# Optimization experiments

Hardware: AMD Instinct MI355X
Metric: run time of the kernel (lower is better)

The kernel has to match this reference:

```python
import jax, jax.numpy as jnp
import numpy as np

CHUNK = 256  # rows of the distance matrix materialized at a time


def _min_sq_dist(x, y):
    """For each point in x [N,3], squared distance to nearest point in y [M,3].
    Computed tile-by-tile via lax.scan so the full [N,M] matrix is never built.
    Matches pytorch3d knn_points(K=1).dists (squared Euclidean)."""
    n = x.shape[0]
    x2 = jnp.sum(x * x, axis=-1)            # [N]
    y2 = jnp.sum(y * y, axis=-1)            # [M]
    xs = x.reshape(n // CHUNK, CHUNK, 3)
    x2s = x2.reshape(n // CHUNK, CHUNK)

    def body(carry, inp):
        xc, x2c = inp                        # [C,3], [C]
        d = x2c[:, None] + y2[None, :] - 2.0 * (xc @ y.T)
        return carry, jnp.min(d, axis=1)     # [C]

    _, mins = jax.lax.scan(body, None, (xs, x2s))
    return mins.reshape(-1)                  # [N]


def setup_inputs() -> dict:
    key = jax.random.key(0)
    k1, k2 = jax.random.split(key)
    pred = jax.random.normal(k1, (131072, 4), dtype=jnp.float32)
    target = jax.random.normal(k2, (131072, 4), dtype=jnp.float32)
    return {"pred": pred, "target": target}


def reference(pred, target):
    loss_weight = 1.0
    p = pred[:, :3]
    t = target[:, :3]
    min_p2t = _min_sq_dist(p, t)   # adv_KNN: pred -> target
    min_t2p = _min_sq_dist(t, p)   # ori_KNN: target -> pred
    chamfer = jnp.mean(min_p2t) + jnp.mean(min_t2p)
    return chamfer * loss_weight
```

## Files before the change

### kernel.cpp

```cpp
#include <hip/hip_runtime.h>


#define G 128
#define GSH 7
#define CCELLS (G * G * G)
#define H 0.1f
#define INVH 10.0f
#define ORIG (-6.4f)
#define NCHUNK (CCELLS / 256)
#define SSTRIDE 2097168u
#define INFB 3.4e38f

__device__ __forceinline__ int cellcoord(float x) {
    int c = (int)floorf((x - ORIG) * INVH);
    return min(max(c, 0), G - 1);
}
__device__ __forceinline__ int cellof(float x, float y, float z) {
    return (cellcoord(z) << (2 * GSH)) + (cellcoord(y) << GSH) + cellcoord(x);
}
__device__ __forceinline__ float axdist(int u, float qc) {
    float lo = ORIG + u * H;
    float dlo = (u == 0) ? 0.0f : lo - qc;
    float dhi = (u == G - 1) ? 0.0f : qc - (lo + H);
    return fmaxf(0.0f, fmaxf(dlo, dhi));
}
__device__ __forceinline__ float scan_run(
    const float4* __restrict__ pts, unsigned int k, unsigned int ke,
    float cx, float cy, float cz, float lbest) {
    for (; k < ke; ++k) {
        float4 ya = pts[k];
        lbest = fminf(lbest, fmaf(cx, ya.x, fmaf(cy, ya.y, fmaf(cz, ya.z, ya.w))));
    }
    return lbest;
}

__global__ __launch_bounds__(256) void hist2_kernel(
    const float4* __restrict__ A, const float4* __restrict__ B,
    unsigned int* __restrict__ counts, int n) {
    int i = blockIdx.x * 256 + threadIdx.x;
    const float4* in = blockIdx.y ? B : A;
    unsigned int* c = counts + blockIdx.y * CCELLS;
    if (i < n) {
        float4 a = in[i];
        atomicAdd(&c[cellof(a.x, a.y, a.z)], 1u);
    }
}

__global__ __launch_bounds__(256) void scan_chunk2_kernel(
    const unsigned int* __restrict__ counts, unsigned int* __restrict__ excl,
    unsigned int* __restrict__ blockSums) {
    __shared__ unsigned int lds[256];
    int cb = blockIdx.x & (NCHUNK - 1);
    int b = blockIdx.x >> 13;
    int g = cb * 256 + threadIdx.x;
    unsigned int v = counts[b * CCELLS + g];
    lds[threadIdx.x] = v;
    __syncthreads();
    for (int off = 1; off < 256; off <<= 1) {
        unsigned int t = (threadIdx.x >= off) ? lds[threadIdx.x - off] : 0u;
        __syncthreads();
        lds[threadIdx.x] += t;
        __syncthreads();
    }
    excl[b * SSTRIDE + g] = lds[threadIdx.x] - v;
    if (threadIdx.x == 255) blockSums[blockIdx.x] = lds[255];
}

__global__ __launch_bounds__(256) void scan_sums2_kernel(
    unsigned int* __restrict__ bs0) {
    unsigned int* bs = bs0 + blockIdx.x * NCHUNK;
    __shared__ unsigned int lds[256];
    int t = threadIdx.x;
    unsigned int s = 0;
    for (int k = 0; k < NCHUNK / 256; ++k) s += bs[t * (NCHUNK / 256) + k];
    lds[t] = s;
    __syncthreads();
    for (int off = 1; off < 256; off <<= 1) {
        unsigned int u = (t >= off) ? lds[t - off] : 0u;
        __syncthreads();
        lds[t] += u;
        __syncthreads();
    }
    unsigned int run = lds[t] - s;
    for (int k = 0; k < NCHUNK / 256; ++k) {
        unsigned int v = bs[t * (NCHUNK / 256) + k];
        bs[t * (NCHUNK / 256) + k] = run;
        run += v;
    }
}

__global__ __launch_bounds__(256) void add_offsets2_kernel(
    unsigned int* __restrict__ excl, unsigned int* __restrict__ next,
    const unsigned int* __restrict__ bs, int n) {
    int cb = blockIdx.x & (NCHUNK - 1);
    int b = blockIdx.x >> 13;
    int g = cb * 256 + threadIdx.x;
    unsigned int v = excl[b * SSTRIDE + g] + bs[blockIdx.x];
    excl[b * SSTRIDE + g] = v;
    next[b * CCELLS + g] = v;
    if (g == 0) excl[b * SSTRIDE + CCELLS] = (unsigned int)n;
}

__global__ __launch_bounds__(256) void scatter2_kernel(
    const float4* __restrict__ A, const float4* __restrict__ B,
    unsigned int* __restrict__ next, float4* __restrict__ sorted, int n) {
    int i = blockIdx.x * 256 + threadIdx.x;
    const float4* in = blockIdx.y ? B : A;
    unsigned int* nx = next + blockIdx.y * CCELLS;
    float4* out = sorted + blockIdx.y * n;
    if (i < n) {
        float4 a = in[i];
        unsigned int slot = atomicAdd(&nx[cellof(a.x, a.y, a.z)], 1u);
        float s = fmaf(a.x, a.x, fmaf(a.y, a.y, a.z * a.z));
        out[slot] = make_float4(a.x, a.y, a.z, s);
    }
}

__global__ __launch_bounds__(256) void nn_pass1_kernel(
    const float4* __restrict__ sortedPT, const unsigned int* __restrict__ startPT,
    int n, unsigned int* __restrict__ wlPT, unsigned int* __restrict__ wbPT,
    unsigned int* __restrict__ cnts, double* __restrict__ acc) {
    int dir = blockIdx.y;
    const float4* Q = sortedPT + (size_t)dir * n;
    const float4* pts = sortedPT + (size_t)(1 - dir) * n;
    const unsigned int* start = startPT + (size_t)(1 - dir) * SSTRIDE;
    unsigned int* wl = wlPT + (size_t)dir * n;
    unsigned int* wb = wbPT + (size_t)dir * n;
    unsigned int* cnt = cnts + dir;

    int i = blockIdx.x * 256 + threadIdx.x;
    float v = 0.0f;
    if (i < n) {
        float4 q = Q[i];
        float cx = -2.0f * q.x, cy = -2.0f * q.y, cz = -2.0f * q.z;
        float q2 = q.w;
        int qx = cellcoord(q.x), qy = cellcoord(q.y), qz = cellcoord(q.z);
        int x0 = max(qx - 1, 0), x1 = min(qx + 1, G - 1);
        unsigned int ss[9], ee[9];
        int idx = 0;
#pragma unroll
        for (int dz = -1; dz <= 1; ++dz) {
            int uz = min(max(qz + dz, 0), G - 1);
#pragma unroll
            for (int dy = -1; dy <= 1; ++dy) {
                int uy = min(max(qy + dy, 0), G - 1);
                unsigned int base = ((unsigned)uz << (2 * GSH)) + ((unsigned)uy << GSH);
                ss[idx] = start[base + x0];
                ee[idx] = start[base + x1 + 1];
                ++idx;
            }
        }
        float best = 3.4e38f;
#pragma unroll
        for (int r = 0; r < 9; ++r) {
            unsigned int k = ss[r], e = ee[r];
            for (; k + 2 <= e; k += 2) {
                float4 ya = pts[k];
                float4 yb = pts[k + 1];
                float ea = fmaf(cx, ya.x, fmaf(cy, ya.y, fmaf(cz, ya.z, ya.w)));
                float eb = fmaf(cx, yb.x, fmaf(cy, yb.y, fmaf(cz, yb.z, yb.w)));
                best = fminf(fminf(best, ea), eb);
            }
            if (k < e) {
                float4 ya = pts[k];
                best = fminf(best, fmaf(cx, ya.x, fmaf(cy, ya.y, fmaf(cz, ya.z, ya.w))));
            }
        }
        float ba = q2 + best;
        float fx = q.x - (ORIG + (float)qx * H);
        float fy = q.y - (ORIG + (float)qy * H);
        float fz = q.z - (ORIG + (float)qz * H);
        float bx = fminf((qx >= 2) ? (fx + H) : INFB,
                         (qx <= G - 3) ? (2.0f * H - fx) : INFB);
        float by = fminf((qy >= 2) ? (fy + H) : INFB,
                         (qy <= G - 3) ? (2.0f * H - fy) : INFB);
        float bz = fminf((qz >= 2) ? (fz + H) : INFB,
                         (qz <= G - 3) ? (2.0f * H - fz) : INFB);
        float bound = fminf(bx, fminf(by, bz)) * 0.99999f;
        if (ba <= bound * bound) {
            v = ba;
        } else {
            unsigned int w = atomicAdd(cnt, 1u);
            wl[w] = (unsigned int)i;
            wb[w] = __float_as_uint(best);
        }
    }
    for (int off = 32; off > 0; off >>= 1) v += __shfl_down(v, off);
    __shared__ float partial[4];
    int lane = threadIdx.x & 63, wid = threadIdx.x >> 6;
    if (lane == 0) partial[wid] = v;
    __syncthreads();
    if (threadIdx.x == 0)
        atomicAdd(acc, (double)((partial[0] + partial[1]) + (partial[2] + partial[3])));
}

__global__ __launch_bounds__(256) void nn_pass2_kernel(
    const float4* __restrict__ sortedPT, const unsigned int* __restrict__ startPT,
    int n, const unsigned int* __restrict__ wlPT, const unsigned int* __restrict__ wbPT,
    const unsigned int* __restrict__ cnts, double* __restrict__ acc) {
    int dir = blockIdx.y;
    const float4* Q = sortedPT + (size_t)dir * n;
    const float4* pts = sortedPT + (size_t)(1 - dir) * n;
    const unsigned int* start = startPT + (size_t)(1 - dir) * SSTRIDE;
    const unsigned int* wl = wlPT + (size_t)dir * n;
    const unsigned int* wb = wbPT + (size_t)dir * n;
    unsigned int m = cnts[dir];

    int lane = threadIdx.x & 63;
    int gwave = (blockIdx.x * 256 + threadIdx.x) >> 6;
    int nwave = gridDim.x * 4;
    float wsum = 0.0f;
    for (unsigned int e = gwave; e < m; e += (unsigned int)nwave) {
        unsigned int qi = wl[e];
        float4 q = Q[qi];
        float cx = -2.0f * q.x, cy = -2.0f * q.y, cz = -2.0f * q.z;
        float q2 = q.w;
        int qx = cellcoord(q.x), qy = cellcoord(q.y), qz = cellcoord(q.z);
        float fx = q.x - (ORIG + (float)qx * H);
        float fy = q.y - (ORIG + (float)qy * H);
        float fz = q.z - (ORIG + (float)qz * H);
        float best = __uint_as_float(wb[e]);
        int Rp = 1;
        int Rb = 2;
        for (;;) {
            int z0 = max(qz - Rb, 0), z1 = min(qz + Rb, G - 1);
            int y0 = max(qy - Rb, 0), y1 = min(qy + Rb, G - 1);
            int x0 = max(qx - Rb, 0), x1 = min(qx + Rb, G - 1);
            int nyr = y1 - y0 + 1;
            int nrows = (z1 - z0 + 1) * nyr;
            float lbest = best;
            for (int r = lane; r < nrows; r += 64) {
                int uz = z0 + r / nyr;
                int uy = y0 + r % nyr;
                int az = uz > qz ? uz - qz : qz - uz;
                int ay = uy > qy ? uy - qy : qy - uy;
                float dz = axdist(uz, q.z), dy = axdist(uy, q.y);
                float rowd2 = fmaf(dz, dz, dy * dy);
                if (rowd2 >= q2 + lbest) continue;
                unsigned int base = ((unsigned)uz << (2 * GSH)) + ((unsigned)uy << GSH);
                if (az <= Rp && ay <= Rp) {
                    int xa1 = qx - Rp - 1;
                    int xb0 = qx + Rp + 1;
                    if (xa1 >= x0)
                        lbest = scan_run(pts, start[base + x0], start[base + xa1 + 1],
                                         cx, cy, cz, lbest);
                    if (xb0 <= x1)
                        lbest = scan_run(pts, start[base + xb0], start[base + x1 + 1],
                                         cx, cy, cz, lbest);
                } else {
                    lbest = scan_run(pts, start[base + x0], start[base + x1 + 1],
                                     cx, cy, cz, lbest);
                }
            }
            for (int off = 32; off > 0; off >>= 1)
                lbest = fminf(lbest, __shfl_xor(lbest, off));
            best = lbest;
            float bx = fminf((qx - Rb >= 1) ? fmaf((float)Rb, H, fx) : INFB,
                             (qx + Rb + 1 <= G - 1) ? ((float)(Rb + 1) * H - fx) : INFB);
            float by = fminf((qy - Rb >= 1) ? fmaf((float)Rb, H, fy) : INFB,
                             (qy + Rb + 1 <= G - 1) ? ((float)(Rb + 1) * H - fy) : INFB);
            float bz = fminf((qz - Rb >= 1) ? fmaf((float)Rb, H, fz) : INFB,
                             (qz + Rb + 1 <= G - 1) ? ((float)(Rb + 1) * H - fz) : INFB);
            float bound = fminf(bx, fminf(by, bz)) * 0.99999f;
            if (q2 + best <= bound * bound || Rb >= G) break;
            Rp = Rb;
            Rb = min(Rb * 2, G);
        }
        wsum += q2 + best;
    }
    if (lane == 0 && wsum != 0.0f) atomicAdd(acc, (double)wsum);
}

__global__ void finalize_kernel(const double* __restrict__ acc,
                                float* __restrict__ out, int n) {
    out[0] = (float)(acc[0] / (double)n);
}

#define SPLIT 16
#define PTS 4
__global__ __launch_bounds__(256) void pack_kernel(
    const float4* __restrict__ in, float4* __restrict__ out, int n) {
    int i = blockIdx.x * 256 + threadIdx.x;
    if (i < n) {
        float4 a = in[i];
        float s = fmaf(a.x, a.x, fmaf(a.y, a.y, a.z * a.z));
        out[i] = make_float4(a.x, a.y, a.z, s);
    }
}
__device__ __forceinline__ unsigned int enc_f32(float f) {
    unsigned int u = __float_as_uint(f);
    return (u & 0x80000000u) ? ~u : (u | 0x80000000u);
}
__device__ __forceinline__ float dec_f32(unsigned int u) {
    u = (u & 0x80000000u) ? (u ^ 0x80000000u) : ~u;
    return __uint_as_float(u);
}
__global__ __launch_bounds__(256) void chamfer_dir_kernel(
    const float4* __restrict__ X, const float4* __restrict__ Y,
    int m, unsigned int* __restrict__ mins) {
    int base = blockIdx.x * (256 * PTS) + threadIdx.x;
    float x2x[PTS], x2y[PTS], x2z[PTS], xw[PTS], mn[PTS];
#pragma unroll
    for (int p = 0; p < PTS; ++p) {
        float4 x = X[base + p * 256];
        x2x[p] = -2.0f * x.x; x2y[p] = -2.0f * x.y; x2z[p] = -2.0f * x.z;
        xw[p] = x.w; mn[p] = 3.4e38f;
    }
    int seglen = m / SPLIT, j0 = blockIdx.y * seglen, j1 = j0 + seglen;
    for (int j = j0; j < j1; j += 8) {
#pragma unroll
        for (int u = 0; u < 8; u += 2) {
            float4 ya = Y[j + u];
            float4 yb = Y[j + u + 1];
#pragma unroll
            for (int p = 0; p < PTS; ++p) {
                float ea = fmaf(x2x[p], ya.x, fmaf(x2y[p], ya.y, fmaf(x2z[p], ya.z, ya.w)));
                float eb = fmaf(x2x[p], yb.x, fmaf(x2y[p], yb.y, fmaf(x2z[p], yb.z, yb.w)));
                mn[p] = fminf(fminf(mn[p], ea), eb);
            }
        }
    }
#pragma unroll
    for (int p = 0; p < PTS; ++p)
        atomicMin(&mins[base + p * 256], enc_f32(xw[p] + mn[p]));
}
__global__ __launch_bounds__(256) void reduce_kernel(
    const unsigned int* __restrict__ mins, int total, double* __restrict__ acc) {
    float s = 0.0f;
    for (int i = blockIdx.x * 256 + threadIdx.x; i < total; i += gridDim.x * 256)
        s += dec_f32(mins[i]);
    for (int off = 32; off > 0; off >>= 1) s += __shfl_down(s, off);
    __shared__ float partial[4];
    int lane = threadIdx.x & 63, wid = threadIdx.x >> 6;
    if (lane == 0) partial[wid] = s;
    __syncthreads();
    if (threadIdx.x == 0)
        atomicAdd(acc, (double)((partial[0] + partial[1]) + (partial[2] + partial[3])));
}

extern "C" void kernel_launch(void* const* d_in, const int* in_sizes, int n_in,
                              void* d_out, int out_size, void* d_ws, size_t ws_size,
                              hipStream_t stream) {
    const float4* pred = (const float4*)d_in[0];
    const float4* targ = (const float4*)d_in[1];
    float* out = (float*)d_out;
    int n = in_sizes[0] / 4;
    int nblk = (n + 255) / 256;

    char* ws = (char*)d_ws;
    double* acc = (double*)ws;
    unsigned int* cnts = (unsigned int*)(ws + 8);

    size_t startB = (size_t)SSTRIDE * 4;
    size_t needGrid = 64 + 2 * startB + 2ull * CCELLS * 4 + 2ull * n * 16
                    + 4ull * n * 4 + 2ull * NCHUNK * 4;

    if (ws_size >= needGrid && n == 131072) {
        char* p = ws + 64;
        unsigned int* startPT = (unsigned int*)p;  p += 2 * startB;
        unsigned int* nextPT = (unsigned int*)p;   p += 2ull * CCELLS * 4;
        float4* sortedPT = (float4*)p;             p += 2ull * n * 16;
        unsigned int* wlPT = (unsigned int*)p;     p += 2ull * n * 4;
        unsigned int* wbPT = (unsigned int*)p;     p += 2ull * n * 4;
        unsigned int* blockSums = (unsigned int*)p;

        hipMemsetAsync(ws, 0, 16, stream);
        hipMemsetAsync(nextPT, 0, 2ull * CCELLS * 4, stream);
        hist2_kernel<<<dim3(nblk, 2), 256, 0, stream>>>(pred, targ, nextPT, n);
        scan_chunk2_kernel<<<2 * NCHUNK, 256, 0, stream>>>(nextPT, startPT, blockSums);
        scan_sums2_kernel<<<2, 256, 0, stream>>>(blockSums);
        add_offsets2_kernel<<<2 * NCHUNK, 256, 0, stream>>>(startPT, nextPT, blockSums, n);
        scatter2_kernel<<<dim3(nblk, 2), 256, 0, stream>>>(pred, targ, nextPT, sortedPT, n);

        nn_pass1_kernel<<<dim3(nblk, 2), 256, 0, stream>>>(
            sortedPT, startPT, n, wlPT, wbPT, cnts, acc);
        nn_pass2_kernel<<<dim3(512, 2), 256, 0, stream>>>(
            sortedPT, startPT, n, wlPT, wbPT, cnts, acc);
    } else {
        hipMemsetAsync(acc, 0, sizeof(double), stream);
        size_t needBF = 64 + 2ull * n * sizeof(float4) + 2ull * n * sizeof(unsigned int);
        if (ws_size >= needBF && (n % (256 * PTS)) == 0 && (n % SPLIT) == 0) {
            float4* P = (float4*)(ws + 64);
            float4* T = P + n;
            unsigned int* minPT = (unsigned int*)(T + n);
            pack_kernel<<<nblk, 256, 0, stream>>>(pred, P, n);
            pack_kernel<<<nblk, 256, 0, stream>>>(targ, T, n);
            hipMemsetAsync(minPT, 0xFF, 2ull * n * sizeof(unsigned int), stream);
            dim3 grid(n / (256 * PTS), SPLIT);
            chamfer_dir_kernel<<<grid, 256, 0, stream>>>(P, T, n, minPT);
            chamfer_dir_kernel<<<grid, 256, 0, stream>>>(T, P, n, minPT + n);
            reduce_kernel<<<256, 256, 0, stream>>>(minPT, 2 * n, acc);
        }
    }
    finalize_kernel<<<1, 1, 0, stream>>>(acc, out, n);
}
```

Measured before the change: 259.6 us.

## Add cell-occupancy bitmask to skip empty rows and dynamic work dequeue in pass2

The histogram kernel now also sets one bit per occupied grid cell in a 64-bit-word bitmap. In the second NN pass, each row of cells is checked against that bitmap, and rows with no points in the x range are skipped before any start-index loads. The strided wave-to-query assignment is replaced by an atomic work queue, so waves pull fallback queries dynamically and uneven search radii balance out. The cost is an extra memset and an atomicOr per point, plus one global atomic per query in pass2.

Result: slower. 455.8 us (+75.6%).

```diff
diff --git a/kernel.cpp b/kernel.cpp
--- a/kernel.cpp
+++ b/kernel.cpp
@@ -9,6 +9,7 @@
 #define ORIG (-6.4f)
 #define NCHUNK (CCELLS / 256)
 #define SSTRIDE 2097168u
+#define OCCW (CCELLS / 64)
 #define INFB 3.4e38f
 
 __device__ __forceinline__ int cellcoord(float x) {
@@ -33,16 +34,23 @@
     }
     return lbest;
 }
+__device__ __forceinline__ unsigned long long rmask(int lo, int hi) {
+    return ((hi - lo == 63) ? ~0ull : (((1ull << (hi - lo + 1)) - 1ull) << lo));
+}
 
 __global__ __launch_bounds__(256) void hist2_kernel(
     const float4* __restrict__ A, const float4* __restrict__ B,
-    unsigned int* __restrict__ counts, int n) {
+    unsigned int* __restrict__ counts, unsigned long long* __restrict__ occ,
+    int n) {
     int i = blockIdx.x * 256 + threadIdx.x;
     const float4* in = blockIdx.y ? B : A;
     unsigned int* c = counts + blockIdx.y * CCELLS;
+    unsigned long long* oc = occ + blockIdx.y * OCCW;
     if (i < n) {
         float4 a = in[i];
-        atomicAdd(&c[cellof(a.x, a.y, a.z)], 1u);
+        int cell = cellof(a.x, a.y, a.z);
+        atomicAdd(&c[cell], 1u);
+        atomicOr(&oc[cell >> 6], 1ull << (cell & 63));
     }
 }
 
@@ -196,21 +204,27 @@
 
 __global__ __launch_bounds__(256) void nn_pass2_kernel(
     const float4* __restrict__ sortedPT, const unsigned int* __restrict__ startPT,
+    const unsigned long long* __restrict__ occPT,
     int n, const unsigned int* __restrict__ wlPT, const unsigned int* __restrict__ wbPT,
-    const unsigned int* __restrict__ cnts, double* __restrict__ acc) {
+    const unsigned int* __restrict__ cnts, unsigned int* __restrict__ deqs,
+    double* __restrict__ acc) {
     int dir = blockIdx.y;
     const float4* Q = sortedPT + (size_t)dir * n;
     const float4* pts = sortedPT + (size_t)(1 - dir) * n;
     const unsigned int* start = startPT + (size_t)(1 - dir) * SSTRIDE;
+    const unsigned long long* occ = occPT + (size_t)(1 - dir) * OCCW;
     const unsigned int* wl = wlPT + (size_t)dir * n;
     const unsigned int* wb = wbPT + (size_t)dir * n;
+    unsigned int* deq = deqs + dir;
     unsigned int m = cnts[dir];
 
     int lane = threadIdx.x & 63;
-    int gwave = (blockIdx.x * 256 + threadIdx.x) >> 6;
-    int nwave = gridDim.x * 4;
     float wsum = 0.0f;
-    for (unsigned int e = gwave; e < m; e += (unsigned int)nwave) {
+    for (;;) {
+        unsigned int e = 0;
+        if (lane == 0) e = atomicAdd(deq, 1u);
+        e = __shfl(e, 0);
+        if (e >= m) break;
         unsigned int qi = wl[e];
         float4 q = Q[qi];
         float cx = -2.0f * q.x, cy = -2.0f * q.y, cz = -2.0f * q.z;
@@ -238,6 +252,13 @@
                 float rowd2 = fmaf(dz, dz, dy * dy);
                 if (rowd2 >= q2 + lbest) continue;
                 unsigned int base = ((unsigned)uz << (2 * GSH)) + ((unsigned)uy << GSH);
+                {
+                    unsigned int w0 = base >> 6;
+                    unsigned long long a = 0;
+                    if (x0 < 64) a = occ[w0] & rmask(x0, min(x1, 63));
+                    if (x1 >= 64) a |= occ[w0 + 1] & rmask(max(x0, 64) - 64, x1 - 64);
+                    if (!a) continue;
+                }
                 if (az <= Rp && ay <= Rp) {
                     int xa1 = qx - Rp - 1;
                     int xb0 = qx + Rp + 1;
@@ -350,23 +371,26 @@
     char* ws = (char*)d_ws;
     double* acc = (double*)ws;
     unsigned int* cnts = (unsigned int*)(ws + 8);
+    unsigned int* deqs = (unsigned int*)(ws + 16);
 
     size_t startB = (size_t)SSTRIDE * 4;
     size_t needGrid = 64 + 2 * startB + 2ull * CCELLS * 4 + 2ull * n * 16
-                    + 4ull * n * 4 + 2ull * NCHUNK * 4;
+                    + 4ull * n * 4 + 2ull * OCCW * 8 + 2ull * NCHUNK * 4;
 
     if (ws_size >= needGrid && n == 131072) {
         char* p = ws + 64;
-        unsigned int* startPT = (unsigned int*)p;  p += 2 * startB;
-        unsigned int* nextPT = (unsigned int*)p;   p += 2ull * CCELLS * 4;
-        float4* sortedPT = (float4*)p;             p += 2ull * n * 16;
-        unsigned int* wlPT = (unsigned int*)p;     p += 2ull * n * 4;
-        unsigned int* wbPT = (unsigned int*)p;     p += 2ull * n * 4;
+        unsigned int* startPT = (unsigned int*)p;        p += 2 * startB;
+        unsigned int* nextPT = (unsigned int*)p;         p += 2ull * CCELLS * 4;
+        float4* sortedPT = (float4*)p;                   p += 2ull * n * 16;
+        unsigned int* wlPT = (unsigned int*)p;           p += 2ull * n * 4;
+        unsigned int* wbPT = (unsigned int*)p;           p += 2ull * n * 4;
+        unsigned long long* occPT = (unsigned long long*)p; p += 2ull * OCCW * 8;
         unsigned int* blockSums = (unsigned int*)p;
 
-        hipMemsetAsync(ws, 0, 16, stream);
+        hipMemsetAsync(ws, 0, 64, stream);
         hipMemsetAsync(nextPT, 0, 2ull * CCELLS * 4, stream);
-        hist2_kernel<<<dim3(nblk, 2), 256, 0, stream>>>(pred, targ, nextPT, n);
+        hipMemsetAsync(occPT, 0, 2ull * OCCW * 8, stream);
+        hist2_kernel<<<dim3(nblk, 2), 256, 0, stream>>>(pred, targ, nextPT, occPT, n);
         scan_chunk2_kernel<<<2 * NCHUNK, 256, 0, stream>>>(nextPT, startPT, blockSums);
         scan_sums2_kernel<<<2, 256, 0, stream>>>(blockSums);
         add_offsets2_kernel<<<2 * NCHUNK, 256, 0, stream>>>(startPT, nextPT, blockSums, n);
@@ -375,7 +399,7 @@
         nn_pass1_kernel<<<dim3(nblk, 2), 256, 0, stream>>>(
             sortedPT, startPT, n, wlPT, wbPT, cnts, acc);
         nn_pass2_kernel<<<dim3(512, 2), 256, 0, stream>>>(
-            sortedPT, startPT, n, wlPT, wbPT, cnts, acc);
+            sortedPT, startPT, occPT, n, wlPT, wbPT, cnts, deqs, acc);
     } else {
         hipMemsetAsync(acc, 0, sizeof(double), stream);
         size_t needBF = 64 + 2ull * n * sizeof(float4) + 2ull * n * sizeof(unsigned int);
```

## Add coarse 32^3 grid for pass-2 nearest-neighbor fallback search

Applied to the files above, without the earlier changes.

Builds a second, coarser uniform grid (32^3 cells of size 0.4) alongside the fine 128^3 grid, with its own histogram, scan and scatter into a reused buffer. The fallback pass-2 search for unresolved queries now walks this coarse grid, growing the search shell by one cell at a time instead of doubling on the fine grid. The aim is fewer cell-start lookups and row iterations for far-away outlier queries. The cost is the extra sort kernels and atomics in the build phase.

After: 316.5 us. 21.9% more time.

```diff
diff --git a/kernel.cpp b/kernel.cpp
--- a/kernel.cpp
+++ b/kernel.cpp
@@ -9,6 +9,15 @@
 #define ORIG (-6.4f)
 #define NCHUNK (CCELLS / 256)
 #define SSTRIDE 2097168u
+
+#define G2 32
+#define GSH2 5
+#define CCELLS2 (G2 * G2 * G2)
+#define H2 0.4f
+#define INVH2 2.5f
+#define NCHUNK2 (CCELLS2 / 256)
+#define SSTRIDE2 32784u
+
 #define INFB 3.4e38f
 
 __device__ __forceinline__ int cellcoord(float x) {
@@ -18,10 +27,17 @@
 __device__ __forceinline__ int cellof(float x, float y, float z) {
     return (cellcoord(z) << (2 * GSH)) + (cellcoord(y) << GSH) + cellcoord(x);
 }
-__device__ __forceinline__ float axdist(int u, float qc) {
-    float lo = ORIG + u * H;
+__device__ __forceinline__ int cellcoord2(float x) {
+    int c = (int)floorf((x - ORIG) * INVH2);
+    return min(max(c, 0), G2 - 1);
+}
+__device__ __forceinline__ int cellof2(float x, float y, float z) {
+    return (cellcoord2(z) << (2 * GSH2)) + (cellcoord2(y) << GSH2) + cellcoord2(x);
+}
+__device__ __forceinline__ float axdist2(int u, float qc) {
+    float lo = ORIG + u * H2;
     float dlo = (u == 0) ? 0.0f : lo - qc;
-    float dhi = (u == G - 1) ? 0.0f : qc - (lo + H);
+    float dhi = (u == G2 - 1) ? 0.0f : qc - (lo + H2);
     return fmaxf(0.0f, fmaxf(dlo, dhi));
 }
 __device__ __forceinline__ float scan_run(
@@ -36,13 +52,16 @@
 
 __global__ __launch_bounds__(256) void hist2_kernel(
     const float4* __restrict__ A, const float4* __restrict__ B,
-    unsigned int* __restrict__ counts, int n) {
+    unsigned int* __restrict__ counts, unsigned int* __restrict__ counts2,
+    int n) {
     int i = blockIdx.x * 256 + threadIdx.x;
     const float4* in = blockIdx.y ? B : A;
     unsigned int* c = counts + blockIdx.y * CCELLS;
+    unsigned int* c2 = counts2 + blockIdx.y * CCELLS2;
     if (i < n) {
         float4 a = in[i];
         atomicAdd(&c[cellof(a.x, a.y, a.z)], 1u);
+        atomicAdd(&c2[cellof2(a.x, a.y, a.z)], 1u);
     }
 }
 
@@ -111,6 +130,69 @@
     if (i < n) {
         float4 a = in[i];
         unsigned int slot = atomicAdd(&nx[cellof(a.x, a.y, a.z)], 1u);
+        float s = fmaf(a.x, a.x, fmaf(a.y, a.y, a.z * a.z));
+        out[slot] = make_float4(a.x, a.y, a.z, s);
+    }
+}
+
+__global__ __launch_bounds__(256) void scan_chunk2c_kernel(
+    const unsigned int* __restrict__ counts2, unsigned int* __restrict__ excl2,
+    unsigned int* __restrict__ blockSums2) {
+    __shared__ unsigned int lds[256];
+    int cb = blockIdx.x & (NCHUNK2 - 1);
+    int b = blockIdx.x >> 7;
+    int g = cb * 256 + threadIdx.x;
+    unsigned int v = counts2[b * CCELLS2 + g];
+    lds[threadIdx.x] = v;
+    __syncthreads();
+    for (int off = 1; off < 256; off <<= 1) {
+        unsigned int t = (threadIdx.x >= off) ? lds[threadIdx.x - off] : 0u;
+        __syncthreads();
+        lds[threadIdx.x] += t;
+        __syncthreads();
+    }
+    excl2[b * SSTRIDE2 + g] = lds[threadIdx.x] - v;
+    if (threadIdx.x == 255) blockSums2[blockIdx.x] = lds[255];
+}
+
+__global__ void scan_sums2c_kernel(unsigned int* __restrict__ bs0) {
+    unsigned int* bs = bs0 + blockIdx.x * NCHUNK2;
+    __shared__ unsigned int lds[NCHUNK2];
+    int t = threadIdx.x;
+    unsigned int v = bs[t];
+    lds[t] = v;
+    __syncthreads();
+    for (int off = 1; off < NCHUNK2; off <<= 1) {
+        unsigned int u = (t >= off) ? lds[t - off] : 0u;
+        __syncthreads();
+        lds[t] += u;
+        __syncthreads();
+    }
+    bs[t] = lds[t] - v;
+}
+
+__global__ __launch_bounds__(256) void add_offsets2c_kernel(
+    unsigned int* __restrict__ excl2, unsigned int* __restrict__ next2,
+    const unsigned int* __restrict__ bs2, int n) {
+    int cb = blockIdx.x & (NCHUNK2 - 1);
+    int b = blockIdx.x >> 7;
+    int g = cb * 256 + threadIdx.x;
+    unsigned int v = excl2[b * SSTRIDE2 + g] + bs2[blockIdx.x];
+    excl2[b * SSTRIDE2 + g] = v;
+    next2[b * CCELLS2 + g] = v;
+    if (g == 0) excl2[b * SSTRIDE2 + CCELLS2] = (unsigned int)n;
+}
+
+__global__ __launch_bounds__(256) void scatter2c_kernel(
+    const float4* __restrict__ A, const float4* __restrict__ B,
+    unsigned int* __restrict__ next2, float4* __restrict__ sortedC, int n) {
+    int i = blockIdx.x * 256 + threadIdx.x;
+    const float4* in = blockIdx.y ? B : A;
+    unsigned int* nx = next2 + blockIdx.y * CCELLS2;
+    float4* out = sortedC + blockIdx.y * n;
+    if (i < n) {
+        float4 a = in[i];
+        unsigned int slot = atomicAdd(&nx[cellof2(a.x, a.y, a.z)], 1u);
         float s = fmaf(a.x, a.x, fmaf(a.y, a.y, a.z * a.z));
         out[slot] = make_float4(a.x, a.y, a.z, s);
     }
@@ -195,13 +277,14 @@
 }
 
 __global__ __launch_bounds__(256) void nn_pass2_kernel(
-    const float4* __restrict__ sortedPT, const unsigned int* __restrict__ startPT,
+    const float4* __restrict__ sortedPT, const float4* __restrict__ sortedC,
+    const unsigned int* __restrict__ startC,
     int n, const unsigned int* __restrict__ wlPT, const unsigned int* __restrict__ wbPT,
     const unsigned int* __restrict__ cnts, double* __restrict__ acc) {
     int dir = blockIdx.y;
     const float4* Q = sortedPT + (size_t)dir * n;
-    const float4* pts = sortedPT + (size_t)(1 - dir) * n;
-    const unsigned int* start = startPT + (size_t)(1 - dir) * SSTRIDE;
+    const float4* pts = sortedC + (size_t)(1 - dir) * n;
+    const unsigned int* start = startC + (size_t)(1 - dir) * SSTRIDE2;
     const unsigned int* wl = wlPT + (size_t)dir * n;
     const unsigned int* wb = wbPT + (size_t)dir * n;
     unsigned int m = cnts[dir];
@@ -215,17 +298,17 @@
         float4 q = Q[qi];
         float cx = -2.0f * q.x, cy = -2.0f * q.y, cz = -2.0f * q.z;
         float q2 = q.w;
-        int qx = cellcoord(q.x), qy = cellcoord(q.y), qz = cellcoord(q.z);
-        float fx = q.x - (ORIG + (float)qx * H);
-        float fy = q.y - (ORIG + (float)qy * H);
-        float fz = q.z - (ORIG + (float)qz * H);
+        int qx = cellcoord2(q.x), qy = cellcoord2(q.y), qz = cellcoord2(q.z);
+        float fx = q.x - (ORIG + (float)qx * H2);
+        float fy = q.y - (ORIG + (float)qy * H2);
+        float fz = q.z - (ORIG + (float)qz * H2);
         float best = __uint_as_float(wb[e]);
-        int Rp = 1;
-        int Rb = 2;
+        int Rp = -1;
+        int Rb = 1;
         for (;;) {
-            int z0 = max(qz - Rb, 0), z1 = min(qz + Rb, G - 1);
-            int y0 = max(qy - Rb, 0), y1 = min(qy + Rb, G - 1);
-            int x0 = max(qx - Rb, 0), x1 = min(qx + Rb, G - 1);
+            int z0 = max(qz - Rb, 0), z1 = min(qz + Rb, G2 - 1);
+            int y0 = max(qy - Rb, 0), y1 = min(qy + Rb, G2 - 1);
+            int x0 = max(qx - Rb, 0), x1 = min(qx + Rb, G2 - 1);
             int nyr = y1 - y0 + 1;
             int nrows = (z1 - z0 + 1) * nyr;
             float lbest = best;
@@ -234,10 +317,10 @@
                 int uy = y0 + r % nyr;
                 int az = uz > qz ? uz - qz : qz - uz;
                 int ay = uy > qy ? uy - qy : qy - uy;
-                float dz = axdist(uz, q.z), dy = axdist(uy, q.y);
+                float dz = axdist2(uz, q.z), dy = axdist2(uy, q.y);
                 float rowd2 = fmaf(dz, dz, dy * dy);
                 if (rowd2 >= q2 + lbest) continue;
-                unsigned int base = ((unsigned)uz << (2 * GSH)) + ((unsigned)uy << GSH);
+                unsigned int base = ((unsigned)uz << (2 * GSH2)) + ((unsigned)uy << GSH2);
                 if (az <= Rp && ay <= Rp) {
                     int xa1 = qx - Rp - 1;
                     int xb0 = qx + Rp + 1;
@@ -255,16 +338,16 @@
             for (int off = 32; off > 0; off >>= 1)
                 lbest = fminf(lbest, __shfl_xor(lbest, off));
             best = lbest;
-            float bx = fminf((qx - Rb >= 1) ? fmaf((float)Rb, H, fx) : INFB,
-                             (qx + Rb + 1 <= G - 1) ? ((float)(Rb + 1) * H - fx) : INFB);
-            float by = fminf((qy - Rb >= 1) ? fmaf((float)Rb, H, fy) : INFB,
-                             (qy + Rb + 1 <= G - 1) ? ((float)(Rb + 1) * H - fy) : INFB);
-            float bz = fminf((qz - Rb >= 1) ? fmaf((float)Rb, H, fz) : INFB,
-                             (qz + Rb + 1 <= G - 1) ? ((float)(Rb + 1) * H - fz) : INFB);
+            float bx = fminf((qx - Rb >= 1) ? fmaf((float)Rb, H2, fx) : INFB,
+                             (qx + Rb + 1 <= G2 - 1) ? ((float)(Rb + 1) * H2 - fx) : INFB);
+            float by = fminf((qy - Rb >= 1) ? fmaf((float)Rb, H2, fy) : INFB,
+                             (qy + Rb + 1 <= G2 - 1) ? ((float)(Rb + 1) * H2 - fy) : INFB);
+            float bz = fminf((qz - Rb >= 1) ? fmaf((float)Rb, H2, fz) : INFB,
+                             (qz + Rb + 1 <= G2 - 1) ? ((float)(Rb + 1) * H2 - fz) : INFB);
             float bound = fminf(bx, fminf(by, bz)) * 0.99999f;
-            if (q2 + best <= bound * bound || Rb >= G) break;
+            if (q2 + best <= bound * bound || Rb >= G2) break;
             Rp = Rb;
-            Rb = min(Rb * 2, G);
+            Rb += 1;
         }
         wsum += q2 + best;
     }
@@ -352,30 +435,40 @@
     unsigned int* cnts = (unsigned int*)(ws + 8);
 
     size_t startB = (size_t)SSTRIDE * 4;
-    size_t needGrid = 64 + 2 * startB + 2ull * CCELLS * 4 + 2ull * n * 16
-                    + 4ull * n * 4 + 2ull * NCHUNK * 4;
+    size_t startB2 = (size_t)SSTRIDE2 * 4;
+    size_t needGrid = 64 + 2 * startB + 2ull * CCELLS * 4 + 2ull * CCELLS2 * 4
+                    + 2 * startB2 + 2ull * n * 16 + 4ull * n * 4
+                    + 2ull * NCHUNK * 4 + 2ull * NCHUNK2 * 4;
 
     if (ws_size >= needGrid && n == 131072) {
         char* p = ws + 64;
         unsigned int* startPT = (unsigned int*)p;  p += 2 * startB;
         unsigned int* nextPT = (unsigned int*)p;   p += 2ull * CCELLS * 4;
+        unsigned int* nextC = (unsigned int*)p;    p += 2ull * CCELLS2 * 4;
+        unsigned int* startC = (unsigned int*)p;   p += 2 * startB2;
         float4* sortedPT = (float4*)p;             p += 2ull * n * 16;
         unsigned int* wlPT = (unsigned int*)p;     p += 2ull * n * 4;
         unsigned int* wbPT = (unsigned int*)p;     p += 2ull * n * 4;
-        unsigned int* blockSums = (unsigned int*)p;
-
-        hipMemsetAsync(ws, 0, 16, stream);
-        hipMemsetAsync(nextPT, 0, 2ull * CCELLS * 4, stream);
-        hist2_kernel<<<dim3(nblk, 2), 256, 0, stream>>>(pred, targ, nextPT, n);
+        unsigned int* blockSums = (unsigned int*)p; p += 2ull * NCHUNK * 4;
+        unsigned int* blockSums2 = (unsigned int*)p;
+        float4* sortedC = (float4*)nextPT;
+
+        hipMemsetAsync(ws, 0, 64, stream);
+        hipMemsetAsync(nextPT, 0, 2ull * CCELLS * 4 + 2ull * CCELLS2 * 4, stream);
+        hist2_kernel<<<dim3(nblk, 2), 256, 0, stream>>>(pred, targ, nextPT, nextC, n);
         scan_chunk2_kernel<<<2 * NCHUNK, 256, 0, stream>>>(nextPT, startPT, blockSums);
         scan_sums2_kernel<<<2, 256, 0, stream>>>(blockSums);
         add_offsets2_kernel<<<2 * NCHUNK, 256, 0, stream>>>(startPT, nextPT, blockSums, n);
         scatter2_kernel<<<dim3(nblk, 2), 256, 0, stream>>>(pred, targ, nextPT, sortedPT, n);
+        scan_chunk2c_kernel<<<2 * NCHUNK2, 256, 0, stream>>>(nextC, startC, blockSums2);
+        scan_sums2c_kernel<<<2, NCHUNK2, 0, stream>>>(blockSums2);
+        add_offsets2c_kernel<<<2 * NCHUNK2, 256, 0, stream>>>(startC, nextC, blockSums2, n);
+        scatter2c_kernel<<<dim3(nblk, 2), 256, 0, stream>>>(pred, targ, nextC, sortedC, n);
 
         nn_pass1_kernel<<<dim3(nblk, 2), 256, 0, stream>>>(
             sortedPT, startPT, n, wlPT, wbPT, cnts, acc);
         nn_pass2_kernel<<<dim3(512, 2), 256, 0, stream>>>(
-            sortedPT, startPT, n, wlPT, wbPT, cnts, acc);
+            sortedPT, sortedC, startC, n, wlPT, wbPT, cnts, acc);
     } else {
         hipMemsetAsync(acc, 0, sizeof(double), stream);
         size_t needBF = 64 + 2ull * n * sizeof(float4) + 2ull * n * sizeof(unsigned int);
```

## Use two-level grid: small fine grid for pass1, coarse grid for pass2 fallback

Applied to the files above, without the earlier changes.

Replaces the single 128^3 fine grid spanning [-6.4,6.4] with a 64^3 fine grid over [-3.2,3.2] for the 3x3x3 first pass, plus a 32^3 coarse grid with 0.4 cell size for the second pass. This shrinks the histogram, scan and offset work over millions of mostly empty cells, and the fine points are clamped to the boundary cells outside the central region. Pass 2 now starts its search radius from the pass-1 best distance and grows it by one coarse cell per step instead of doubling, and it launches twice as many blocks. The cost is a second scatter into a second sorted copy, plus more points clamped into edge cells, which can send more queries to the slower pass 2.

Result: slower. 736.4 us (+183.7%).

```diff
diff --git a/kernel.cpp b/kernel.cpp
--- a/kernel.cpp
+++ b/kernel.cpp
@@ -1,27 +1,44 @@
 #include <hip/hip_runtime.h>
 
 
-#define G 128
-#define GSH 7
-#define CCELLS (G * G * G)
-#define H 0.1f
-#define INVH 10.0f
-#define ORIG (-6.4f)
-#define NCHUNK (CCELLS / 256)
-#define SSTRIDE 2097168u
+#define GF 64
+#define GSHF 6
+#define CCF (GF * GF * GF)
+#define HF 0.1f
+#define INVHF 10.0f
+#define ORIGF (-3.2f)
+#define NCHF (CCF / 256)
+#define SSF 262160u
+
+#define G2 32
+#define GSH2 5
+#define CC2 (G2 * G2 * G2)
+#define H2 0.4f
+#define INVH2 2.5f
+#define ORIG2 (-6.4f)
+#define NCH2 (CC2 / 256)
+#define SS2 32784u
+
 #define INFB 3.4e38f
 
-__device__ __forceinline__ int cellcoord(float x) {
-    int c = (int)floorf((x - ORIG) * INVH);
-    return min(max(c, 0), G - 1);
-}
-__device__ __forceinline__ int cellof(float x, float y, float z) {
-    return (cellcoord(z) << (2 * GSH)) + (cellcoord(y) << GSH) + cellcoord(x);
-}
-__device__ __forceinline__ float axdist(int u, float qc) {
-    float lo = ORIG + u * H;
+__device__ __forceinline__ int cellcoordF(float x) {
+    int c = (int)floorf((x - ORIGF) * INVHF);
+    return min(max(c, 0), GF - 1);
+}
+__device__ __forceinline__ int cellofF(float x, float y, float z) {
+    return (cellcoordF(z) << (2 * GSHF)) + (cellcoordF(y) << GSHF) + cellcoordF(x);
+}
+__device__ __forceinline__ int cellcoord2(float x) {
+    int c = (int)floorf((x - ORIG2) * INVH2);
+    return min(max(c, 0), G2 - 1);
+}
+__device__ __forceinline__ int cellof2(float x, float y, float z) {
+    return (cellcoord2(z) << (2 * GSH2)) + (cellcoord2(y) << GSH2) + cellcoord2(x);
+}
+__device__ __forceinline__ float axdist2(int u, float qc) {
+    float lo = ORIG2 + u * H2;
     float dlo = (u == 0) ? 0.0f : lo - qc;
-    float dhi = (u == G - 1) ? 0.0f : qc - (lo + H);
+    float dhi = (u == G2 - 1) ? 0.0f : qc - (lo + H2);
     return fmaxf(0.0f, fmaxf(dlo, dhi));
 }
 __device__ __forceinline__ float scan_run(
@@ -36,24 +53,45 @@
 
 __global__ __launch_bounds__(256) void hist2_kernel(
     const float4* __restrict__ A, const float4* __restrict__ B,
-    unsigned int* __restrict__ counts, int n) {
+    unsigned int* __restrict__ countsF, unsigned int* __restrict__ countsC,
+    int n) {
     int i = blockIdx.x * 256 + threadIdx.x;
     const float4* in = blockIdx.y ? B : A;
-    unsigned int* c = counts + blockIdx.y * CCELLS;
+    unsigned int* cF = countsF + (size_t)blockIdx.y * CCF;
+    unsigned int* cC = countsC + (size_t)blockIdx.y * CC2;
     if (i < n) {
         float4 a = in[i];
-        atomicAdd(&c[cellof(a.x, a.y, a.z)], 1u);
-    }
-}
-
-__global__ __launch_bounds__(256) void scan_chunk2_kernel(
-    const unsigned int* __restrict__ counts, unsigned int* __restrict__ excl,
-    unsigned int* __restrict__ blockSums) {
+        atomicAdd(&cF[cellofF(a.x, a.y, a.z)], 1u);
+        atomicAdd(&cC[cellof2(a.x, a.y, a.z)], 1u);
+    }
+}
+
+__global__ __launch_bounds__(256) void scan_chunk_all_kernel(
+    const unsigned int* __restrict__ countsF, unsigned int* __restrict__ exclF,
+    unsigned int* __restrict__ bsF,
+    const unsigned int* __restrict__ countsC, unsigned int* __restrict__ exclC,
+    unsigned int* __restrict__ bsC) {
     __shared__ unsigned int lds[256];
-    int cb = blockIdx.x & (NCHUNK - 1);
-    int b = blockIdx.x >> 13;
-    int g = cb * 256 + threadIdx.x;
-    unsigned int v = counts[b * CCELLS + g];
+    int bid = blockIdx.x;
+    const unsigned int* cnt;
+    unsigned int* excl;
+    unsigned int* bsp;
+    int g;
+    if (bid < 2 * NCHF) {
+        int b = bid >> 10, cb = bid & (NCHF - 1);
+        g = cb * 256 + threadIdx.x;
+        cnt = countsF + (size_t)b * CCF;
+        excl = exclF + (size_t)b * SSF;
+        bsp = bsF + bid;
+    } else {
+        int b2 = bid - 2 * NCHF;
+        int b = b2 >> 7, cb = b2 & (NCH2 - 1);
+        g = cb * 256 + threadIdx.x;
+        cnt = countsC + (size_t)b * CC2;
+        excl = exclC + (size_t)b * SS2;
+        bsp = bsC + b2;
+    }
+    unsigned int v = cnt[g];
     lds[threadIdx.x] = v;
     __syncthreads();
     for (int off = 1; off < 256; off <<= 1) {
@@ -62,68 +100,99 @@
         lds[threadIdx.x] += t;
         __syncthreads();
     }
-    excl[b * SSTRIDE + g] = lds[threadIdx.x] - v;
-    if (threadIdx.x == 255) blockSums[blockIdx.x] = lds[255];
-}
-
-__global__ __launch_bounds__(256) void scan_sums2_kernel(
-    unsigned int* __restrict__ bs0) {
-    unsigned int* bs = bs0 + blockIdx.x * NCHUNK;
+    excl[g] = lds[threadIdx.x] - v;
+    if (threadIdx.x == 255) *bsp = lds[255];
+}
+
+__global__ __launch_bounds__(256) void scan_sums_all_kernel(
+    unsigned int* __restrict__ bsF, unsigned int* __restrict__ bsC) {
+    int b = blockIdx.x;
+    unsigned int* bs = (b < 2) ? bsF + b * NCHF : bsC + (b - 2) * NCH2;
+    int len = (b < 2) ? NCHF : NCH2;
     __shared__ unsigned int lds[256];
-    int t = threadIdx.x;
-    unsigned int s = 0;
-    for (int k = 0; k < NCHUNK / 256; ++k) s += bs[t * (NCHUNK / 256) + k];
-    lds[t] = s;
+    __shared__ unsigned int carrySh;
+    if (threadIdx.x == 0) carrySh = 0;
     __syncthreads();
-    for (int off = 1; off < 256; off <<= 1) {
-        unsigned int u = (t >= off) ? lds[t - off] : 0u;
+    for (int base = 0; base < len; base += 256) {
+        int idx = base + threadIdx.x;
+        unsigned int v = (idx < len) ? bs[idx] : 0u;
+        lds[threadIdx.x] = v;
         __syncthreads();
-        lds[t] += u;
+        for (int off = 1; off < 256; off <<= 1) {
+            unsigned int t = (threadIdx.x >= off) ? lds[threadIdx.x - off] : 0u;
+            __syncthreads();
+            lds[threadIdx.x] += t;
+            __syncthreads();
+        }
+        unsigned int carry = carrySh;
+        if (idx < len) bs[idx] = carry + lds[threadIdx.x] - v;
         __syncthreads();
-    }
-    unsigned int run = lds[t] - s;
-    for (int k = 0; k < NCHUNK / 256; ++k) {
-        unsigned int v = bs[t * (NCHUNK / 256) + k];
-        bs[t * (NCHUNK / 256) + k] = run;
-        run += v;
-    }
-}
-
-__global__ __launch_bounds__(256) void add_offsets2_kernel(
-    unsigned int* __restrict__ excl, unsigned int* __restrict__ next,
-    const unsigned int* __restrict__ bs, int n) {
-    int cb = blockIdx.x & (NCHUNK - 1);
-    int b = blockIdx.x >> 13;
-    int g = cb * 256 + threadIdx.x;
-    unsigned int v = excl[b * SSTRIDE + g] + bs[blockIdx.x];
-    excl[b * SSTRIDE + g] = v;
-    next[b * CCELLS + g] = v;
-    if (g == 0) excl[b * SSTRIDE + CCELLS] = (unsigned int)n;
-}
-
-__global__ __launch_bounds__(256) void scatter2_kernel(
+        if (threadIdx.x == 255) carrySh = carry + lds[255];
+        __syncthreads();
+    }
+}
+
+__global__ __launch_bounds__(256) void add_offsets_all_kernel(
+    unsigned int* __restrict__ exclF, unsigned int* __restrict__ nextF,
+    const unsigned int* __restrict__ bsF,
+    unsigned int* __restrict__ exclC, unsigned int* __restrict__ nextC,
+    const unsigned int* __restrict__ bsC, int n) {
+    int bid = blockIdx.x;
+    unsigned int* excl;
+    unsigned int* next;
+    unsigned int add;
+    int g, cells;
+    if (bid < 2 * NCHF) {
+        int b = bid >> 10, cb = bid & (NCHF - 1);
+        g = cb * 256 + threadIdx.x;
+        excl = exclF + (size_t)b * SSF;
+        next = nextF + (size_t)b * CCF;
+        add = bsF[bid];
+        cells = CCF;
+    } else {
+        int b2 = bid - 2 * NCHF;
+        int b = b2 >> 7, cb = b2 & (NCH2 - 1);
+        g = cb * 256 + threadIdx.x;
+        excl = exclC + (size_t)b * SS2;
+        next = nextC + (size_t)b * CC2;
+        add = bsC[b2];
+        cells = CC2;
+    }
+    unsigned int v = excl[g] + add;
+    excl[g] = v;
+    next[g] = v;
+    if (g == 0) excl[cells] = (unsigned int)n;
+}
+
+__global__ __launch_bounds__(256) void scatter_all_kernel(
     const float4* __restrict__ A, const float4* __restrict__ B,
-    unsigned int* __restrict__ next, float4* __restrict__ sorted, int n) {
+    unsigned int* __restrict__ nextF, unsigned int* __restrict__ nextC,
+    float4* __restrict__ sortedF, float4* __restrict__ sortedC, int n) {
     int i = blockIdx.x * 256 + threadIdx.x;
     const float4* in = blockIdx.y ? B : A;
-    unsigned int* nx = next + blockIdx.y * CCELLS;
-    float4* out = sorted + blockIdx.y * n;
+    unsigned int* nxF = nextF + (size_t)blockIdx.y * CCF;
+    unsigned int* nxC = nextC + (size_t)blockIdx.y * CC2;
+    float4* outF = sortedF + (size_t)blockIdx.y * n;
+    float4* outC = sortedC + (size_t)blockIdx.y * n;
     if (i < n) {
         float4 a = in[i];
-        unsigned int slot = atomicAdd(&nx[cellof(a.x, a.y, a.z)], 1u);
         float s = fmaf(a.x, a.x, fmaf(a.y, a.y, a.z * a.z));
-        out[slot] = make_float4(a.x, a.y, a.z, s);
+        float4 pt = make_float4(a.x, a.y, a.z, s);
+        unsigned int sF = atomicAdd(&nxF[cellofF(a.x, a.y, a.z)], 1u);
+        outF[sF] = pt;
+        unsigned int sC = atomicAdd(&nxC[cellof2(a.x, a.y, a.z)], 1u);
+        outC[sC] = pt;
     }
 }
 
 __global__ __launch_bounds__(256) void nn_pass1_kernel(
-    const float4* __restrict__ sortedPT, const unsigned int* __restrict__ startPT,
+    const float4* __restrict__ sortedF, const unsigned int* __restrict__ startF,
     int n, unsigned int* __restrict__ wlPT, unsigned int* __restrict__ wbPT,
     unsigned int* __restrict__ cnts, double* __restrict__ acc) {
     int dir = blockIdx.y;
-    const float4* Q = sortedPT + (size_t)dir * n;
-    const float4* pts = sortedPT + (size_t)(1 - dir) * n;
-    const unsigned int* start = startPT + (size_t)(1 - dir) * SSTRIDE;
+    const float4* Q = sortedF + (size_t)dir * n;
+    const float4* pts = sortedF + (size_t)(1 - dir) * n;
+    const unsigned int* start = startF + (size_t)(1 - dir) * SSF;
     unsigned int* wl = wlPT + (size_t)dir * n;
     unsigned int* wb = wbPT + (size_t)dir * n;
     unsigned int* cnt = cnts + dir;
@@ -134,23 +203,23 @@
         float4 q = Q[i];
         float cx = -2.0f * q.x, cy = -2.0f * q.y, cz = -2.0f * q.z;
         float q2 = q.w;
-        int qx = cellcoord(q.x), qy = cellcoord(q.y), qz = cellcoord(q.z);
-        int x0 = max(qx - 1, 0), x1 = min(qx + 1, G - 1);
+        int qx = cellcoordF(q.x), qy = cellcoordF(q.y), qz = cellcoordF(q.z);
+        int x0 = max(qx - 1, 0), x1 = min(qx + 1, GF - 1);
         unsigned int ss[9], ee[9];
         int idx = 0;
 #pragma unroll
         for (int dz = -1; dz <= 1; ++dz) {
-            int uz = min(max(qz + dz, 0), G - 1);
+            int uz = min(max(qz + dz, 0), GF - 1);
 #pragma unroll
             for (int dy = -1; dy <= 1; ++dy) {
-                int uy = min(max(qy + dy, 0), G - 1);
-                unsigned int base = ((unsigned)uz << (2 * GSH)) + ((unsigned)uy << GSH);
+                int uy = min(max(qy + dy, 0), GF - 1);
+                unsigned int base = ((unsigned)uz << (2 * GSHF)) + ((unsigned)uy << GSHF);
                 ss[idx] = start[base + x0];
                 ee[idx] = start[base + x1 + 1];
                 ++idx;
             }
         }
-        float best = 3.4e38f;
+        float best = INFB;
 #pragma unroll
         for (int r = 0; r < 9; ++r) {
             unsigned int k = ss[r], e = ee[r];
@@ -167,15 +236,15 @@
             }
         }
         float ba = q2 + best;
-        float fx = q.x - (ORIG + (float)qx * H);
-        float fy = q.y - (ORIG + (float)qy * H);
-        float fz = q.z - (ORIG + (float)qz * H);
-        float bx = fminf((qx >= 2) ? (fx + H) : INFB,
-                         (qx <= G - 3) ? (2.0f * H - fx) : INFB);
-        float by = fminf((qy >= 2) ? (fy + H) : INFB,
-                         (qy <= G - 3) ? (2.0f * H - fy) : INFB);
-        float bz = fminf((qz >= 2) ? (fz + H) : INFB,
-                         (qz <= G - 3) ? (2.0f * H - fz) : INFB);
+        float fx = q.x - (ORIGF + (float)qx * HF);
+        float fy = q.y - (ORIGF + (float)qy * HF);
+        float fz = q.z - (ORIGF + (float)qz * HF);
+        float bx = fminf((qx >= 2) ? (fx + HF) : INFB,
+                         (qx <= GF - 3) ? (2.0f * HF - fx) : INFB);
+        float by = fminf((qy >= 2) ? (fy + HF) : INFB,
+                         (qy <= GF - 3) ? (2.0f * HF - fy) : INFB);
+        float bz = fminf((qz >= 2) ? (fz + HF) : INFB,
+                         (qz <= GF - 3) ? (2.0f * HF - fz) : INFB);
         float bound = fminf(bx, fminf(by, bz)) * 0.99999f;
         if (ba <= bound * bound) {
             v = ba;
@@ -195,13 +264,14 @@
 }
 
 __global__ __launch_bounds__(256) void nn_pass2_kernel(
-    const float4* __restrict__ sortedPT, const unsigned int* __restrict__ startPT,
+    const float4* __restrict__ sortedF, const float4* __restrict__ sortedC,
+    const unsigned int* __restrict__ startC,
     int n, const unsigned int* __restrict__ wlPT, const unsigned int* __restrict__ wbPT,
     const unsigned int* __restrict__ cnts, double* __restrict__ acc) {
     int dir = blockIdx.y;
-    const float4* Q = sortedPT + (size_t)dir * n;
-    const float4* pts = sortedPT + (size_t)(1 - dir) * n;
-    const unsigned int* start = startPT + (size_t)(1 - dir) * SSTRIDE;
+    const float4* Q = sortedF + (size_t)dir * n;
+    const float4* pts = sortedC + (size_t)(1 - dir) * n;
+    const unsigned int* start = startC + (size_t)(1 - dir) * SS2;
     const unsigned int* wl = wlPT + (size_t)dir * n;
     const unsigned int* wb = wbPT + (size_t)dir * n;
     unsigned int m = cnts[dir];
@@ -215,17 +285,19 @@
         float4 q = Q[qi];
         float cx = -2.0f * q.x, cy = -2.0f * q.y, cz = -2.0f * q.z;
         float q2 = q.w;
-        int qx = cellcoord(q.x), qy = cellcoord(q.y), qz = cellcoord(q.z);
-        float fx = q.x - (ORIG + (float)qx * H);
-        float fy = q.y - (ORIG + (float)qy * H);
-        float fz = q.z - (ORIG + (float)qz * H);
+        int qx = cellcoord2(q.x), qy = cellcoord2(q.y), qz = cellcoord2(q.z);
+        float fx = q.x - (ORIG2 + (float)qx * H2);
+        float fy = q.y - (ORIG2 + (float)qy * H2);
+        float fz = q.z - (ORIG2 + (float)qz * H2);
         float best = __uint_as_float(wb[e]);
-        int Rp = 1;
-        int Rb = 2;
+        float D = sqrtf(fminf(q2 + best, 16.0f));
+        int Rb = (int)ceilf(D * INVH2);
+        Rb = min(max(Rb, 1), 4);
+        int Rp = -1;
         for (;;) {
-            int z0 = max(qz - Rb, 0), z1 = min(qz + Rb, G - 1);
-            int y0 = max(qy - Rb, 0), y1 = min(qy + Rb, G - 1);
-            int x0 = max(qx - Rb, 0), x1 = min(qx + Rb, G - 1);
+            int z0 = max(qz - Rb, 0), z1 = min(qz + Rb, G2 - 1);
+            int y0 = max(qy - Rb, 0), y1 = min(qy + Rb, G2 - 1);
+            int x0 = max(qx - Rb, 0), x1 = min(qx + Rb, G2 - 1);
             int nyr = y1 - y0 + 1;
             int nrows = (z1 - z0 + 1) * nyr;
             float lbest = best;
@@ -234,10 +306,10 @@
                 int uy = y0 + r % nyr;
                 int az = uz > qz ? uz - qz : qz - uz;
                 int ay = uy > qy ? uy - qy : qy - uy;
-                float dz = axdist(uz, q.z), dy = axdist(uy, q.y);
+                float dz = axdist2(uz, q.z), dy = axdist2(uy, q.y);
                 float rowd2 = fmaf(dz, dz, dy * dy);
                 if (rowd2 >= q2 + lbest) continue;
-                unsigned int base = ((unsigned)uz << (2 * GSH)) + ((unsigned)uy << GSH);
+                unsigned int base = ((unsigned)uz << (2 * GSH2)) + ((unsigned)uy << GSH2);
                 if (az <= Rp && ay <= Rp) {
                     int xa1 = qx - Rp - 1;
                     int xb0 = qx + Rp + 1;
@@ -255,16 +327,16 @@
             for (int off = 32; off > 0; off >>= 1)
                 lbest = fminf(lbest, __shfl_xor(lbest, off));
             best = lbest;
-            float bx = fminf((qx - Rb >= 1) ? fmaf((float)Rb, H, fx) : INFB,
-                             (qx + Rb + 1 <= G - 1) ? ((float)(Rb + 1) * H - fx) : INFB);
-            float by = fminf((qy - Rb >= 1) ? fmaf((float)Rb, H, fy) : INFB,
-                             (qy + Rb + 1 <= G - 1) ? ((float)(Rb + 1) * H - fy) : INFB);
-            float bz = fminf((qz - Rb >= 1) ? fmaf((float)Rb, H, fz) : INFB,
-                             (qz + Rb + 1 <= G - 1) ? ((float)(Rb + 1) * H - fz) : INFB);
+            float bx = fminf((qx - Rb >= 1) ? fmaf((float)Rb, H2, fx) : INFB,
+                             (qx + Rb + 1 <= G2 - 1) ? ((float)(Rb + 1) * H2 - fx) : INFB);
+            float by = fminf((qy - Rb >= 1) ? fmaf((float)Rb, H2, fy) : INFB,
+                             (qy + Rb + 1 <= G2 - 1) ? ((float)(Rb + 1) * H2 - fy) : INFB);
+            float bz = fminf((qz - Rb >= 1) ? fmaf((float)Rb, H2, fz) : INFB,
+                             (qz + Rb + 1 <= G2 - 1) ? ((float)(Rb + 1) * H2 - fz) : INFB);
             float bound = fminf(bx, fminf(by, bz)) * 0.99999f;
-            if (q2 + best <= bound * bound || Rb >= G) break;
+            if (q2 + best <= bound * bound || Rb >= G2) break;
             Rp = Rb;
-            Rb = min(Rb * 2, G);
+            Rb = min(Rb + 1, G2);
         }
         wsum += q2 + best;
     }
@@ -304,7 +376,7 @@
     for (int p = 0; p < PTS; ++p) {
         float4 x = X[base + p * 256];
         x2x[p] = -2.0f * x.x; x2y[p] = -2.0f * x.y; x2z[p] = -2.0f * x.z;
-        xw[p] = x.w; mn[p] = 3.4e38f;
+        xw[p] = x.w; mn[p] = INFB;
     }
     int seglen = m / SPLIT, j0 = blockIdx.y * seglen, j1 = j0 + seglen;
     for (int j = j0; j < j1; j += 8) {
@@ -351,31 +423,40 @@
     double* acc = (double*)ws;
     unsigned int* cnts = (unsigned int*)(ws + 8);
 
-    size_t startB = (size_t)SSTRIDE * 4;
-    size_t needGrid = 64 + 2 * startB + 2ull * CCELLS * 4 + 2ull * n * 16
-                    + 4ull * n * 4 + 2ull * NCHUNK * 4;
+    size_t startFB = (size_t)SSF * 4;
+    size_t startCB = (size_t)SS2 * 4;
+    size_t needGrid = 64 + 2 * startFB + 2 * startCB + 2ull * CCF * 4
+                    + 2ull * CC2 * 4 + 4ull * n * 16 + 4ull * n * 4
+                    + 2ull * NCHF * 4 + 2ull * NCH2 * 4;
 
     if (ws_size >= needGrid && n == 131072) {
         char* p = ws + 64;
-        unsigned int* startPT = (unsigned int*)p;  p += 2 * startB;
-        unsigned int* nextPT = (unsigned int*)p;   p += 2ull * CCELLS * 4;
-        float4* sortedPT = (float4*)p;             p += 2ull * n * 16;
+        unsigned int* startF = (unsigned int*)p;   p += 2 * startFB;
+        unsigned int* startC = (unsigned int*)p;   p += 2 * startCB;
+        unsigned int* nextF = (unsigned int*)p;    p += 2ull * CCF * 4;
+        unsigned int* nextC = (unsigned int*)p;    p += 2ull * CC2 * 4;
+        float4* sortedF = (float4*)p;              p += 2ull * n * 16;
+        float4* sortedC = (float4*)p;              p += 2ull * n * 16;
         unsigned int* wlPT = (unsigned int*)p;     p += 2ull * n * 4;
         unsigned int* wbPT = (unsigned int*)p;     p += 2ull * n * 4;
-        unsigned int* blockSums = (unsigned int*)p;
-
-        hipMemsetAsync(ws, 0, 16, stream);
-        hipMemsetAsync(nextPT, 0, 2ull * CCELLS * 4, stream);
-        hist2_kernel<<<dim3(nblk, 2), 256, 0, stream>>>(pred, targ, nextPT, n);
-        scan_chunk2_kernel<<<2 * NCHUNK, 256, 0, stream>>>(nextPT, startPT, blockSums);
-        scan_sums2_kernel<<<2, 256, 0, stream>>>(blockSums);
-        add_offsets2_kernel<<<2 * NCHUNK, 256, 0, stream>>>(startPT, nextPT, blockSums, n);
-        scatter2_kernel<<<dim3(nblk, 2), 256, 0, stream>>>(pred, targ, nextPT, sortedPT, n);
+        unsigned int* bsF = (unsigned int*)p;      p += 2ull * NCHF * 4;
+        unsigned int* bsC = (unsigned int*)p;
+
+        hipMemsetAsync(ws, 0, 64, stream);
+        hipMemsetAsync(nextF, 0, 2ull * CCF * 4 + 2ull * CC2 * 4, stream);
+        hist2_kernel<<<dim3(nblk, 2), 256, 0, stream>>>(pred, targ, nextF, nextC, n);
+        scan_chunk_all_kernel<<<2 * NCHF + 2 * NCH2, 256, 0, stream>>>(
+            nextF, startF, bsF, nextC, startC, bsC);
+        scan_sums_all_kernel<<<4, 256, 0, stream>>>(bsF, bsC);
+        add_offsets_all_kernel<<<2 * NCHF + 2 * NCH2, 256, 0, stream>>>(
+            startF, nextF, bsF, startC, nextC, bsC, n);
+        scatter_all_kernel<<<dim3(nblk, 2), 256, 0, stream>>>(
+            pred, targ, nextF, nextC, sortedF, sortedC, n);
 
         nn_pass1_kernel<<<dim3(nblk, 2), 256, 0, stream>>>(
-            sortedPT, startPT, n, wlPT, wbPT, cnts, acc);
-        nn_pass2_kernel<<<dim3(512, 2), 256, 0, stream>>>(
-            sortedPT, startPT, n, wlPT, wbPT, cnts, acc);
+            sortedF, startF, n, wlPT, wbPT, cnts, acc);
+        nn_pass2_kernel<<<dim3(1024, 2), 256, 0, stream>>>(
+            sortedF, sortedC, startC, n, wlPT, wbPT, cnts, acc);
     } else {
         hipMemsetAsync(acc, 0, sizeof(double), stream);
         size_t needBF = 64 + 2ull * n * sizeof(float4) + 2ull * n * sizeof(unsigned int);
```
